# Performance work log

Hardware: AMD Instinct MI355X
Metric: run time of the kernel (lower is better)

The kernel has to match this reference:

```python
import jax, jax.numpy as jnp
from jax import lax
import numpy as np

N_STATE, N_CTRL, T, B = 64, 32, 50, 256
N = N_STATE + N_CTRL


def setup_inputs() -> dict:
    key = jax.random.key(0)
    k1, k2, k3, k4, k5, k6 = jax.random.split(key, 6)
    # SPD cost Hessians so Qt_uu stays invertible through the Riccati recursion
    A = jax.random.normal(k1, (T, B, N, N), jnp.float32) / np.float32(np.sqrt(N))
    C = jnp.einsum('tbij,tbkj->tbik', A, A) + jnp.eye(N, dtype=jnp.float32)
    c = 0.1 * jax.random.normal(k2, (T, B, N), jnp.float32)
    # mildly contractive dynamics to keep the 50-step recursion well-scaled
    F = jax.random.normal(k3, (T, B, N_STATE, N), jnp.float32) * np.float32(0.5 / np.sqrt(N))
    x_init = jax.random.normal(k4, (B, N_STATE), jnp.float32)
    current_x = jax.random.normal(k5, (T, B, N_STATE), jnp.float32)
    current_u = jax.random.normal(k6, (T, B, N_CTRL), jnp.float32)
    return {'x_init': x_init, 'C': C, 'c': c, 'F': F,
            'current_x': current_x, 'current_u': current_u}


def _lqr(x_init, C, c, F, current_x, current_u):
    ns = current_x.shape[-1]
    # delta_space linearized cost: c_back[t] = C[t] @ [x_t; u_t] + c[t]
    xut = jnp.concatenate([current_x, current_u], axis=-1)          # [T,B,N]
    c_back = jnp.einsum('tbij,tbj->tbi', C, xut) + c                # [T,B,N]

    def bwd_step(carry, inp):
        V, v = carry                                                # [B,ns,ns],[B,ns]
        Ct, ct, Ft = inp
        FtT = jnp.swapaxes(Ft, -1, -2)                              # [B,N,ns]
        Qt = Ct + FtT @ V @ Ft                                      # [B,N,N]
        qt = ct + jnp.einsum('bij,bi->bj', Ft, v)                   # Ft^T v
        Q_xx = Qt[:, :ns, :ns]; Q_xu = Qt[:, :ns, ns:]
        Q_ux = Qt[:, ns:, :ns]; Q_uu = Qt[:, ns:, ns:]
        q_x = qt[:, :ns]; q_u = qt[:, ns:]
        Kt = -jnp.linalg.solve(Q_uu, Q_ux)                          # [B,nc,ns]
        kt = -jnp.linalg.solve(Q_uu, q_u[..., None])[..., 0]        # [B,nc]
        KtT = jnp.swapaxes(Kt, -1, -2)
        Vn = Q_xx + Q_xu @ Kt + KtT @ Q_ux + KtT @ Q_uu @ Kt
        vn = (q_x + jnp.einsum('bij,bj->bi', Q_xu, kt)
              + jnp.einsum('bji,bj->bi', Kt, q_u)
              + jnp.einsum('bji,bjk,bk->bi', Kt, Q_uu, kt))
        return (Vn, vn), (Kt, kt)

    Bsz = x_init.shape[0]
    V0 = jnp.zeros((Bsz, ns, ns), C.dtype)
    v0 = jnp.zeros((Bsz, ns), C.dtype)
    # scan from t = T-1 down to 0 (V0 = 0 makes the last step Qt = C[T-1])
    _, (K_rev, k_rev) = lax.scan(bwd_step, (V0, v0),
                                 (C[::-1], c_back[::-1], F[::-1]))
    K = K_rev[::-1]   # [T,B,nc,ns], gain at time t
    k = k_rev[::-1]   # [T,B,nc]

    # forward rollout (single line-search iter, alpha = 1)
    x_ref_next = jnp.concatenate([current_x[1:], jnp.zeros_like(current_x[:1])], 0)

    def fwd_step(carry, inp):
        xt, dxt = carry
        Kt, kt, ut, Ft, xr = inp
        new_ut = jnp.einsum('bij,bj->bi', Kt, dxt) + ut + kt
        new_xut = jnp.concatenate([xt, new_ut], axis=-1)
        x_next = jnp.einsum('bij,bj->bi', Ft, new_xut)
        return (x_next, x_next - xr), (xt, new_ut)

    _, (new_x, new_u) = lax.scan(fwd_step, (x_init, jnp.zeros_like(x_init)),
                                 (K, k, current_u, F, x_ref_next))
    return new_x, new_u


def reference(x_init, C, c, F, current_x, current_u):
    return _lqr(x_init, C, c, F, current_x, current_u)
```

## Files before the change

### kernel.cpp

```cpp
#include <hip/hip_runtime.h>
#include <cstddef>

#define NS 64
#define NC 32
#define NN 96
#define TT 50
#define BB 256
#define NT 512

#define VS 68
#define QS 104
#define FS 104
#define AS 104

#define OFF_V    0
#define OFF_Q    4352
#define OFF_F    14336
#define OFF_M    20992
#define OFF_A    27648
#define OFF_PROW 30976
#define OFF_PCOL 31184
#define OFF_XUT  31248
#define OFF_CV   31344
#define OFF_QT   31440
#define OFF_VV   31536
#define LDS_FLOATS 31600

extern "C" __global__ __launch_bounds__(NT, 1)
void lqr_fused(const float* __restrict__ x_init,
               const float* __restrict__ Cg, const float* __restrict__ cg,
               const float* __restrict__ Fg, const float* __restrict__ cxg,
               const float* __restrict__ cug, float* __restrict__ Kg,
               float* __restrict__ kg, float* __restrict__ out)
{
    extern __shared__ float sm[];
    float* Vb   = sm + OFF_V;
    float* Qb   = sm + OFF_Q;
    float* Fb   = sm + OFF_F;
    float* Mb   = sm + OFF_M;
    float* Ab   = sm + OFF_A;
    float* prow = sm + OFF_PROW;
    float* pcol = sm + OFF_PCOL;
    float* xut  = sm + OFF_XUT;
    float* cv   = sm + OFF_CV;
    float* qtv  = sm + OFF_QT;
    float* vv   = sm + OFF_VV;

    const int b   = blockIdx.x;
    const int tid = threadIdx.x;

    float4 creg[5];
    float4 fnew[3];
    float  xreg = 0.f, cvreg = 0.f;

    {
        const int t = TT - 1;
        const float* Fsrc = Fg + ((size_t)t * BB + b) * (NS * NN);
        #pragma unroll
        for (int rr = 0; rr < 3; ++rr) {
            int f = tid + NT * rr;
            float4 val = ((const float4*)Fsrc)[f];
            int row = f / 24, c4 = f % 24;
            *(float4*)&Fb[row * FS + 4 * c4] = val;
        }
        const float* Csrc = Cg + ((size_t)t * BB + b) * (NN * NN);
        #pragma unroll
        for (int rr = 0; rr < 4; ++rr) creg[rr] = ((const float4*)Csrc)[tid + NT * rr];
        if (tid < 256) creg[4] = ((const float4*)Csrc)[tid + 2048];

        if (tid < NN) {
            xut[tid] = (tid < NS) ? cxg[((size_t)t * BB + b) * NS + tid]
                                  : cug[((size_t)t * BB + b) * NC + (tid - NS)];
            cv[tid] = cg[((size_t)t * BB + b) * NN + tid];
        }
        for (int e = tid; e < NS * VS; e += NT) Vb[e] = 0.f;
        if (tid < NS) vv[tid] = 0.f;
    }
    __syncthreads();

    for (int t = TT - 1; t >= 0; --t) {
        #pragma unroll
        for (int rr = 0; rr < 5; ++rr) {
            if (rr < 4 || tid < 256) {
                int f = tid + NT * rr;
                int row = f / 24, c4 = f % 24;
                *(float4*)&Qb[row * QS + 4 * c4] = creg[rr];
            }
        }
        if (t > 0) {
            const float* Cs = Cg + ((size_t)(t - 1) * BB + b) * (NN * NN);
            #pragma unroll
            for (int rr = 0; rr < 4; ++rr) creg[rr] = ((const float4*)Cs)[tid + NT * rr];
            if (tid < 256) creg[4] = ((const float4*)Cs)[tid + 2048];
            const float* Fs = Fg + ((size_t)(t - 1) * BB + b) * (NS * NN);
            #pragma unroll
            for (int rr = 0; rr < 3; ++rr) fnew[rr] = ((const float4*)Fs)[tid + NT * rr];
            if (tid < NN) {
                xreg  = (tid < NS) ? cxg[((size_t)(t - 1) * BB + b) * NS + tid]
                                   : cug[((size_t)(t - 1) * BB + b) * NC + (tid - NS)];
                cvreg = cg[((size_t)(t - 1) * BB + b) * NN + tid];
            }
        }

        {
            const int ty = tid >> 4, tx = tid & 15;
            const int i0 = 2 * ty, j0 = 6 * tx;
            float acc[2][6];
            #pragma unroll
            for (int a = 0; a < 2; ++a)
                #pragma unroll
                for (int q = 0; q < 6; ++q) acc[a][q] = 0.f;
            for (int k = 0; k < NS; k += 4) {
                float4 v0 = *(const float4*)&Vb[i0 * VS + k];
                float4 v1 = *(const float4*)&Vb[(i0 + 1) * VS + k];
                #pragma unroll
                for (int dk = 0; dk < 4; ++dk) {
                    float2 f0 = *(const float2*)&Fb[(k + dk) * FS + j0];
                    float2 f1 = *(const float2*)&Fb[(k + dk) * FS + j0 + 2];
                    float2 f2 = *(const float2*)&Fb[(k + dk) * FS + j0 + 4];
                    float fv[6] = {f0.x, f0.y, f1.x, f1.y, f2.x, f2.y};
                    float a0k = (&v0.x)[dk], a1k = (&v1.x)[dk];
                    #pragma unroll
                    for (int q = 0; q < 6; ++q) {
                        acc[0][q] += a0k * fv[q];
                        acc[1][q] += a1k * fv[q];
                    }
                }
            }
            #pragma unroll
            for (int a = 0; a < 2; ++a) {
                *(float2*)&Mb[(i0 + a) * FS + j0]     = make_float2(acc[a][0], acc[a][1]);
                *(float2*)&Mb[(i0 + a) * FS + j0 + 2] = make_float2(acc[a][2], acc[a][3]);
                *(float2*)&Mb[(i0 + a) * FS + j0 + 4] = make_float2(acc[a][4], acc[a][5]);
            }
        }
        __syncthreads();

        if (tid < NN) {
            const int j = tid;
            float s0 = cv[j], s1 = 0.f;
            for (int i = 0; i < NN; i += 2) {
                s0 += Qb[i * QS + j] * xut[i];
                s1 += Qb[(i + 1) * QS + j] * xut[i + 1];
            }
            for (int i = 0; i < NS; i += 2) {
                s0 += Fb[i * FS + j] * vv[i];
                s1 += Fb[(i + 1) * FS + j] * vv[i + 1];
            }
            float s = s0 + s1;
            qtv[j] = s;
            if (j >= NS) Ab[(j - NS) * AS + 96] = s;
        }
        __syncthreads();

        {
            const int ty = tid >> 4, tx = tid & 15;
            const int a0 = 3 * ty, b0 = 6 * tx;
            float acc[3][6];
            #pragma unroll
            for (int dr = 0; dr < 3; ++dr) {
                float2 q0 = *(const float2*)&Qb[(a0 + dr) * QS + b0];
                float2 q1 = *(const float2*)&Qb[(a0 + dr) * QS + b0 + 2];
                float2 q2 = *(const float2*)&Qb[(a0 + dr) * QS + b0 + 4];
                acc[dr][0] = q0.x; acc[dr][1] = q0.y; acc[dr][2] = q1.x;
                acc[dr][3] = q1.y; acc[dr][4] = q2.x; acc[dr][5] = q2.y;
            }
            for (int i = 0; i < NS; ++i) {
                float fa0 = Fb[i * FS + a0];
                float fa1 = Fb[i * FS + a0 + 1];
                float fa2 = Fb[i * FS + a0 + 2];
                float2 m0 = *(const float2*)&Mb[i * FS + b0];
                float2 m1 = *(const float2*)&Mb[i * FS + b0 + 2];
                float2 m2 = *(const float2*)&Mb[i * FS + b0 + 4];
                float mb[6] = {m0.x, m0.y, m1.x, m1.y, m2.x, m2.y};
                float fa[3] = {fa0, fa1, fa2};
                #pragma unroll
                for (int dr = 0; dr < 3; ++dr)
                    #pragma unroll
                    for (int q = 0; q < 6; ++q) acc[dr][q] += fa[dr] * mb[q];
            }
            #pragma unroll
            for (int dr = 0; dr < 3; ++dr) {
                *(float2*)&Qb[(a0 + dr) * QS + b0]     = make_float2(acc[dr][0], acc[dr][1]);
                *(float2*)&Qb[(a0 + dr) * QS + b0 + 2] = make_float2(acc[dr][2], acc[dr][3]);
                *(float2*)&Qb[(a0 + dr) * QS + b0 + 4] = make_float2(acc[dr][4], acc[dr][5]);
                int row = a0 + dr;
                if (row >= NS) {
                    int rr = row - NS;
                    #pragma unroll
                    for (int q = 0; q < 6; ++q) {
                        int c  = b0 + q;
                        int ac = (c < NS) ? (c + NC) : (c - NS);
                        Ab[rr * AS + ac] = acc[dr][q];
                    }
                }
            }
        }
        __syncthreads();

        if (t > 0) {
            #pragma unroll
            for (int rr = 0; rr < 3; ++rr) {
                int f = tid + NT * rr;
                int row = f / 24, c4 = f % 24;
                *(float4*)&Fb[row * FS + 4 * c4] = fnew[rr];
            }
            if (tid < NN) { xut[tid] = xreg; cv[tid] = cvreg; }
        }

        float myinv;
        {
            const int g = tid & 15, r = tid >> 4;
            const int jlo = 6 * g;
            float a[6], a6;
            #pragma unroll
            for (int q = 0; q < 6; ++q) a[q] = Ab[r * AS + jlo + q];
            a6 = (g == 15) ? Ab[r * AS + 96] : 0.f;
            myinv = 0.f;
            if (r == 0) {
                #pragma unroll
                for (int q = 0; q < 6; ++q) prow[jlo + q] = a[q];
                if (g == 15) prow[96] = a6;
            }
            if (g == 0) pcol[r] = a[0];
            __syncthreads();

            #pragma unroll
            for (int p = 0; p < NC; ++p) {
                const int buf = (p & 1) * 104, nb = ((p + 1) & 1) * 104;
                const int cbuf = (p & 1) * 32, cnb = ((p + 1) & 1) * 32;
                float piv = prow[buf + p];
                float pc  = pcol[cbuf + r];
                float r0  = __builtin_amdgcn_rcpf(piv);
                r0 = r0 * (2.f - piv * r0);
                float fac = (r == p) ? 0.f : pc * r0;
                float2 w0 = *(const float2*)&prow[buf + jlo];
                float2 w1 = *(const float2*)&prow[buf + jlo + 2];
                float2 w2 = *(const float2*)&prow[buf + jlo + 4];
                float w6  = prow[buf + 96];
                a[0] -= fac * w0.x; a[1] -= fac * w0.y;
                a[2] -= fac * w1.x; a[3] -= fac * w1.y;
                a[4] -= fac * w2.x; a[5] -= fac * w2.y;
                a6   -= fac * w6;
                myinv = (r == p) ? r0 : myinv;
                if (p < NC - 1) {
                    const int np = p + 1;
                    if (g == np / 6) pcol[cnb + r] = a[np % 6];
                    if (r == np) {
                        *(float2*)&prow[nb + jlo]     = make_float2(a[0], a[1]);
                        *(float2*)&prow[nb + jlo + 2] = make_float2(a[2], a[3]);
                        *(float2*)&prow[nb + jlo + 4] = make_float2(a[4], a[5]);
                        if (g == 15) prow[nb + 96] = a6;
                    }
                }
                __syncthreads();
            }
            #pragma unroll
            for (int q = 0; q < 6; ++q) {
                int j = jlo + q;
                if (j >= NC) Ab[r * AS + j] = -a[q] * myinv;
            }
            if (g == 15) Ab[r * AS + 96] = -a6 * myinv;
        }
        __syncthreads();

        {
            float* Kt = Kg + ((size_t)t * BB + b) * (NC * NS);
            for (int e = tid; e < NC * NS; e += NT) {
                int m = e >> 6, x = e & 63;
                Kt[e] = Ab[m * AS + 32 + x];
            }
            if (tid < NC) kg[((size_t)t * BB + b) * NC + tid] = Ab[tid * AS + 96];
        }
        {
            const int ty = tid >> 4, tx = tid & 15;
            const int i0 = 2 * ty, j0 = 4 * tx;
            float acc[2][4];
            #pragma unroll
            for (int di = 0; di < 2; ++di) {
                float4 q = *(const float4*)&Qb[(i0 + di) * QS + j0];
                acc[di][0] = q.x; acc[di][1] = q.y; acc[di][2] = q.z; acc[di][3] = q.w;
            }
            for (int m = 0; m < NC; ++m) {
                float2 qx = *(const float2*)&Qb[(NS + m) * QS + i0];
                float4 kk = *(const float4*)&Ab[m * AS + 32 + j0];
                float kv[4] = {kk.x, kk.y, kk.z, kk.w};
                #pragma unroll
                for (int dj = 0; dj < 4; ++dj) {
                    acc[0][dj] += qx.x * kv[dj];
                    acc[1][dj] += qx.y * kv[dj];
                }
            }
            #pragma unroll
            for (int di = 0; di < 2; ++di)
                *(float4*)&Vb[(i0 + di) * VS + j0] =
                    make_float4(acc[di][0], acc[di][1], acc[di][2], acc[di][3]);
        }
        if (tid < NS) {
            float s0 = qtv[tid], s1 = 0.f;
            for (int m = 0; m < NC; m += 2) {
                s0 += Qb[(NS + m) * QS + tid] * Ab[m * AS + 96];
                s1 += Qb[(NS + m + 1) * QS + tid] * Ab[(m + 1) * AS + 96];
            }
            vv[tid] = s0 + s1;
        }
        __syncthreads();
    }

    {
        float* xpp = sm;
        float* dxs = sm + 192;
        float* out_x = out;
        float* out_u = out + (size_t)TT * BB * NS;

        if (tid < NS) { xpp[tid] = x_init[(size_t)b * NS + tid]; dxs[tid] = 0.f; }
        __syncthreads();

        const int mK = tid >> 3, qK = tid & 7;
        const int iF = tid >> 2, qF = tid & 3;
        float kr[8], fr[24];
        if (tid < 256) {
            const float* Ksrc = Kg + (size_t)b * (NC * NS);
            #pragma unroll
            for (int xx = 0; xx < 8; ++xx) kr[xx] = Ksrc[mK * NS + qK + 8 * xx];
            const float* Fsrc = Fg + (size_t)b * (NS * NN);
            #pragma unroll
            for (int jj = 0; jj < 24; ++jj) fr[jj] = Fsrc[iF * NN + qF + 4 * jj];
        }

        for (int t = 0; t < TT; ++t) {
            const int cur = (t & 1) * 96, nxt = ((t + 1) & 1) * 96;
            const int curd = (t & 1) * 64, nxtd = ((t + 1) & 1) * 64;
            float krn[8], frn[24];
            if (tid < 256) {
                int tn = (t + 1 < TT) ? (t + 1) : t;
                const float* Ksrc = Kg + ((size_t)tn * BB + b) * (NC * NS);
                #pragma unroll
                for (int xx = 0; xx < 8; ++xx) krn[xx] = Ksrc[mK * NS + qK + 8 * xx];
                const float* Fsrc = Fg + ((size_t)tn * BB + b) * (NS * NN);
                #pragma unroll
                for (int jj = 0; jj < 24; ++jj) frn[jj] = Fsrc[iF * NN + qF + 4 * jj];
            }
            if (tid < NS) out_x[((size_t)t * BB + b) * NS + tid] = xpp[cur + tid];
            if (tid < 256) {
                float s = 0.f;
                #pragma unroll
                for (int xx = 0; xx < 8; ++xx) s += kr[xx] * dxs[curd + qK + 8 * xx];
                s += __shfl_down(s, 4); s += __shfl_down(s, 2); s += __shfl_down(s, 1);
                if (qK == 0) {
                    float un = s + cug[((size_t)t * BB + b) * NC + mK]
                                 + kg[((size_t)t * BB + b) * NC + mK];
                    xpp[cur + NS + mK] = un;
                    out_u[((size_t)t * BB + b) * NC + mK] = un;
                }
            }
            __syncthreads();
            if (tid < 256) {
                float s = 0.f;
                #pragma unroll
                for (int jj = 0; jj < 24; ++jj) s += fr[jj] * xpp[cur + qF + 4 * jj];
                s += __shfl_down(s, 2); s += __shfl_down(s, 1);
                if (qF == 0) {
                    float xr = (t + 1 < TT) ? cxg[((size_t)(t + 1) * BB + b) * NS + iF] : 0.f;
                    xpp[nxt + iF] = s;
                    dxs[nxtd + iF] = s - xr;
                }
                #pragma unroll
                for (int xx = 0; xx < 8; ++xx) kr[xx] = krn[xx];
                #pragma unroll
                for (int jj = 0; jj < 24; ++jj) fr[jj] = frn[jj];
            }
            __syncthreads();
        }
    }
}

extern "C" void kernel_launch(void* const* d_in, const int* in_sizes, int n_in,
                              void* d_out, int out_size, void* d_ws, size_t ws_size,
                              hipStream_t stream)
{
    const float* x_init = (const float*)d_in[0];
    const float* Cg     = (const float*)d_in[1];
    const float* cg     = (const float*)d_in[2];
    const float* Fg     = (const float*)d_in[3];
    const float* cxg    = (const float*)d_in[4];
    const float* cug    = (const float*)d_in[5];
    float* out = (float*)d_out;

    float* Kg = (float*)d_ws;
    float* kg = Kg + (size_t)TT * BB * NC * NS;

    hipFuncSetAttribute((const void*)lqr_fused,
                        hipFuncAttributeMaxDynamicSharedMemorySize,
                        LDS_FLOATS * 4);

    lqr_fused<<<BB, NT, LDS_FLOATS * 4, stream>>>(x_init, Cg, cg, Fg, cxg, cug,
                                                  Kg, kg, out);
}
```

Measured before the change: 1.884 ms.

## Block Gauss-Jordan elimination four pivots per barrier and use LDS-only barriers

```diff
diff --git a/kernel.cpp b/kernel.cpp
--- a/kernel.cpp
+++ b/kernel.cpp
@@ -18,13 +18,22 @@
 #define OFF_F    14336
 #define OFF_M    20992
 #define OFF_A    27648
-#define OFF_PROW 30976
-#define OFF_PCOL 31184
-#define OFF_XUT  31248
-#define OFF_CV   31344
-#define OFF_QT   31440
-#define OFF_VV   31536
-#define LDS_FLOATS 31600
+#define OFF_PR   30976
+#define OFF_PC   31808
+#define OFF_XUT  32064
+#define OFF_CV   32160
+#define OFF_QT   32256
+#define OFF_VV   32352
+#define LDS_FLOATS 32416
+
+__device__ __forceinline__ void bar() {
+    asm volatile("s_waitcnt lgkmcnt(0)\n\ts_barrier" ::: "memory");
+}
+
+__device__ __forceinline__ float frcp(float x) {
+    float r = __builtin_amdgcn_rcpf(x);
+    return r * (2.f - x * r);
+}
 
 extern "C" __global__ __launch_bounds__(NT, 1)
 void lqr_fused(const float* __restrict__ x_init,
@@ -39,8 +48,8 @@
     float* Fb   = sm + OFF_F;
     float* Mb   = sm + OFF_M;
     float* Ab   = sm + OFF_A;
-    float* prow = sm + OFF_PROW;
-    float* pcol = sm + OFF_PCOL;
+    float* PRb  = sm + OFF_PR;
+    float* PCb  = sm + OFF_PC;
     float* xut  = sm + OFF_XUT;
     float* cv   = sm + OFF_CV;
     float* qtv  = sm + OFF_QT;
@@ -76,7 +85,7 @@
         for (int e = tid; e < NS * VS; e += NT) Vb[e] = 0.f;
         if (tid < NS) vv[tid] = 0.f;
     }
-    __syncthreads();
+    bar();
 
     for (int t = TT - 1; t >= 0; --t) {
         #pragma unroll
@@ -134,24 +143,29 @@
                 *(float2*)&Mb[(i0 + a) * FS + j0 + 4] = make_float2(acc[a][4], acc[a][5]);
             }
         }
-        __syncthreads();
-
-        if (tid < NN) {
-            const int j = tid;
-            float s0 = cv[j], s1 = 0.f;
-            for (int i = 0; i < NN; i += 2) {
-                s0 += Qb[i * QS + j] * xut[i];
-                s1 += Qb[(i + 1) * QS + j] * xut[i + 1];
-            }
-            for (int i = 0; i < NS; i += 2) {
-                s0 += Fb[i * FS + j] * vv[i];
-                s1 += Fb[(i + 1) * FS + j] * vv[i + 1];
-            }
-            float s = s0 + s1;
-            qtv[j] = s;
-            if (j >= NS) Ab[(j - NS) * AS + 96] = s;
-        }
-        __syncthreads();
+        bar();
+
+        if (tid < 384) {
+            const int j = tid >> 2, s = tid & 3;
+            float acc = (s == 0) ? cv[j] : 0.f;
+            #pragma unroll 4
+            for (int it = 0; it < 24; ++it) {
+                int i = 4 * it + s;
+                acc += Qb[i * QS + j] * xut[i];
+            }
+            #pragma unroll 4
+            for (int it = 0; it < 16; ++it) {
+                int i = 4 * it + s;
+                acc += Fb[i * FS + j] * vv[i];
+            }
+            acc += __shfl_down(acc, 1);
+            acc += __shfl_down(acc, 2);
+            if (s == 0) {
+                qtv[j] = acc;
+                if (j >= NS) Ab[(j - NS) * AS + 96] = acc;
+            }
+        }
+        bar();
 
         {
             const int ty = tid >> 4, tx = tid & 15;
@@ -196,7 +210,7 @@
                 }
             }
         }
-        __syncthreads();
+        bar();
 
         if (t > 0) {
             #pragma unroll
@@ -208,7 +222,7 @@
             if (tid < NN) { xut[tid] = xreg; cv[tid] = cvreg; }
         }
 
-        float myinv;
+        float myinv = 0.f;
         {
             const int g = tid & 15, r = tid >> 4;
             const int jlo = 6 * g;
@@ -216,44 +230,115 @@
             #pragma unroll
             for (int q = 0; q < 6; ++q) a[q] = Ab[r * AS + jlo + q];
             a6 = (g == 15) ? Ab[r * AS + 96] : 0.f;
-            myinv = 0.f;
-            if (r == 0) {
-                #pragma unroll
-                for (int q = 0; q < 6; ++q) prow[jlo + q] = a[q];
-                if (g == 15) prow[96] = a6;
-            }
-            if (g == 0) pcol[r] = a[0];
-            __syncthreads();
-
-            #pragma unroll
-            for (int p = 0; p < NC; ++p) {
-                const int buf = (p & 1) * 104, nb = ((p + 1) & 1) * 104;
-                const int cbuf = (p & 1) * 32, cnb = ((p + 1) & 1) * 32;
-                float piv = prow[buf + p];
-                float pc  = pcol[cbuf + r];
-                float r0  = __builtin_amdgcn_rcpf(piv);
-                r0 = r0 * (2.f - piv * r0);
-                float fac = (r == p) ? 0.f : pc * r0;
-                float2 w0 = *(const float2*)&prow[buf + jlo];
-                float2 w1 = *(const float2*)&prow[buf + jlo + 2];
-                float2 w2 = *(const float2*)&prow[buf + jlo + 4];
-                float w6  = prow[buf + 96];
-                a[0] -= fac * w0.x; a[1] -= fac * w0.y;
-                a[2] -= fac * w1.x; a[3] -= fac * w1.y;
-                a[4] -= fac * w2.x; a[5] -= fac * w2.y;
-                a6   -= fac * w6;
-                myinv = (r == p) ? r0 : myinv;
-                if (p < NC - 1) {
-                    const int np = p + 1;
-                    if (g == np / 6) pcol[cnb + r] = a[np % 6];
-                    if (r == np) {
-                        *(float2*)&prow[nb + jlo]     = make_float2(a[0], a[1]);
-                        *(float2*)&prow[nb + jlo + 2] = make_float2(a[2], a[3]);
-                        *(float2*)&prow[nb + jlo + 4] = make_float2(a[4], a[5]);
-                        if (g == 15) prow[nb + 96] = a6;
+            if (r < 4) {
+                #pragma unroll
+                for (int q = 0; q < 6; ++q) PRb[r * 104 + jlo + q] = a[q];
+                if (g == 15) PRb[r * 104 + 96] = a6;
+            }
+            if (g == 0) {
+                #pragma unroll
+                for (int i = 0; i < 4; ++i) PCb[i * 32 + r] = a[i];
+            }
+            bar();
+
+            for (int rnd = 0; rnd < 8; ++rnd) {
+                const int p0 = 4 * rnd;
+                const float* PRc = PRb + (rnd & 1) * 416;
+                const float* PCc = PCb + (rnd & 1) * 128;
+                float* PRn = PRb + ((rnd + 1) & 1) * 416;
+                float* PCn = PCb + ((rnd + 1) & 1) * 128;
+
+                float W0p0 = PRc[0 * 104 + p0 + 0];
+                float W0p1 = PRc[0 * 104 + p0 + 1];
+                float W0p2 = PRc[0 * 104 + p0 + 2];
+                float W0p3 = PRc[0 * 104 + p0 + 3];
+                float R1p1 = PRc[1 * 104 + p0 + 1];
+                float R1p2 = PRc[1 * 104 + p0 + 2];
+                float R1p3 = PRc[1 * 104 + p0 + 3];
+                float R2p2 = PRc[2 * 104 + p0 + 2];
+                float R2p3 = PRc[2 * 104 + p0 + 3];
+                float R3p3 = PRc[3 * 104 + p0 + 3];
+                float C0p1 = PCc[0 * 32 + p0 + 1];
+                float C0p2 = PCc[0 * 32 + p0 + 2];
+                float C0p3 = PCc[0 * 32 + p0 + 3];
+                float C1p2 = PCc[1 * 32 + p0 + 2];
+                float C1p3 = PCc[1 * 32 + p0 + 3];
+                float C2p3 = PCc[2 * 32 + p0 + 3];
+
+                float r0 = frcp(W0p0);
+                float g1 = C0p1 * r0;
+                float W1p1 = R1p1 - g1 * W0p1;
+                float r1 = frcp(W1p1);
+                float W1p2 = R1p2 - g1 * W0p2;
+                float W1p3 = R1p3 - g1 * W0p3;
+                float h0 = C0p2 * r0;
+                float h1 = (C1p2 - h0 * W0p1) * r1;
+                float W2p2 = R2p2 - h0 * W0p2 - h1 * W1p2;
+                float r2 = frcp(W2p2);
+                float W2p3 = R2p3 - h0 * W0p3 - h1 * W1p3;
+                float k0 = C0p3 * r0;
+                float k1 = (C1p3 - k0 * W0p1) * r1;
+                float k2 = (C2p3 - k0 * W0p2 - k1 * W1p2) * r2;
+                float W3p3 = R3p3 - k0 * W0p3 - k1 * W1p3 - k2 * W2p3;
+                float r3 = frcp(W3p3);
+
+                float c0 = PCc[0 * 32 + r];
+                float c1 = PCc[1 * 32 + r];
+                float c2 = PCc[2 * 32 + r];
+                float c3 = PCc[3 * 32 + r];
+                float fac0 = (r == p0)     ? 0.f : c0 * r0;
+                float a1   = c1 - fac0 * W0p1;
+                float fac1 = (r == p0 + 1) ? 0.f : a1 * r1;
+                float a2   = c2 - fac0 * W0p2 - fac1 * W1p2;
+                float fac2 = (r == p0 + 2) ? 0.f : a2 * r2;
+                float a3   = c3 - fac0 * W0p3 - fac1 * W1p3 - fac2 * W2p3;
+                float fac3 = (r == p0 + 3) ? 0.f : a3 * r3;
+
+                if (r == p0)     myinv = r0;
+                if (r == p0 + 1) myinv = r1;
+                if (r == p0 + 2) myinv = r2;
+                if (r == p0 + 3) myinv = r3;
+
+                #pragma unroll
+                for (int q = 0; q < 6; ++q) {
+                    float w0  = PRc[0 * 104 + jlo + q];
+                    float w1r = PRc[1 * 104 + jlo + q];
+                    float w2r = PRc[2 * 104 + jlo + q];
+                    float w3r = PRc[3 * 104 + jlo + q];
+                    float w1 = w1r - g1 * w0;
+                    float w2 = w2r - h0 * w0 - h1 * w1;
+                    float w3 = w3r - k0 * w0 - k1 * w1 - k2 * w2;
+                    a[q] -= fac0 * w0;
+                    a[q] -= fac1 * w1;
+                    a[q] -= fac2 * w2;
+                    a[q] -= fac3 * w3;
+                }
+                if (g == 15) {
+                    float w0  = PRc[0 * 104 + 96];
+                    float w1 = PRc[1 * 104 + 96] - g1 * w0;
+                    float w2 = PRc[2 * 104 + 96] - h0 * w0 - h1 * w1;
+                    float w3 = PRc[3 * 104 + 96] - k0 * w0 - k1 * w1 - k2 * w2;
+                    a6 -= fac0 * w0;
+                    a6 -= fac1 * w1;
+                    a6 -= fac2 * w2;
+                    a6 -= fac3 * w3;
+                }
+
+                if (rnd < 7) {
+                    const int np0 = p0 + 4;
+                    if (r >= np0 && r < np0 + 4) {
+                        float* dst = PRn + (r - np0) * 104;
+                        #pragma unroll
+                        for (int q = 0; q < 6; ++q) dst[jlo + q] = a[q];
+                        if (g == 15) dst[96] = a6;
                     }
-                }
-                __syncthreads();
+                    #pragma unroll
+                    for (int q = 0; q < 6; ++q) {
+                        int c = jlo + q;
+                        if (c >= np0 && c < np0 + 4) PCn[(c - np0) * 32 + r] = a[q];
+                    }
+                    bar();
+                }
             }
             #pragma unroll
             for (int q = 0; q < 6; ++q) {
@@ -262,7 +347,7 @@
             }
             if (g == 15) Ab[r * AS + 96] = -a6 * myinv;
         }
-        __syncthreads();
+        bar();
 
         {
             float* Kt = Kg + ((size_t)t * BB + b) * (NC * NS);
@@ -304,8 +389,11 @@
             }
             vv[tid] = s0 + s1;
         }
-        __syncthreads();
+        bar();
     }
+
+    asm volatile("s_waitcnt vmcnt(0)" ::: "memory");
+    __syncthreads();
 
     {
         float* xpp = sm;
@@ -314,7 +402,7 @@
         float* out_u = out + (size_t)TT * BB * NS;
 
         if (tid < NS) { xpp[tid] = x_init[(size_t)b * NS + tid]; dxs[tid] = 0.f; }
-        __syncthreads();
+        bar();
 
         const int mK = tid >> 3, qK = tid & 7;
         const int iF = tid >> 2, qF = tid & 3;
@@ -354,7 +442,7 @@
                     out_u[((size_t)t * BB + b) * NC + mK] = un;
                 }
             }
-            __syncthreads();
+            bar();
             if (tid < 256) {
                 float s = 0.f;
                 #pragma unroll
@@ -370,7 +458,7 @@
                 #pragma unroll
                 for (int jj = 0; jj < 24; ++jj) fr[jj] = frn[jj];
             }
-            __syncthreads();
+            bar();
         }
     }
 }
```

New measurement: 1.907 ms. About the same (+1.2%).
